# Kernel optimization log

Measured on AMD Instinct MI355X. Metric: run time of the kernel, lower is better.

Reference implementation:

```python
import jax, jax.numpy as jnp
import numpy as np
import math

B, N, M = 4, 2048, 2048
DIM_Q = DIM_K = DIM_V = 1024
H = 16

def setup_inputs() -> dict:
    key = jax.random.key(0)
    ks = jax.random.split(key, 10)
    s = 0.02
    return {
        "Q": jax.random.normal(ks[0], (B, N, DIM_Q), jnp.float32),
        "K": jax.random.normal(ks[1], (B, M, DIM_K), jnp.float32),
        "Wq": jax.random.normal(ks[2], (DIM_V, DIM_Q), jnp.float32) * s,
        "bq": jax.random.normal(ks[3], (DIM_V,), jnp.float32) * s,
        "Wk": jax.random.normal(ks[4], (DIM_V, DIM_K), jnp.float32) * s,
        "bk": jax.random.normal(ks[5], (DIM_V,), jnp.float32) * s,
        "Wv": jax.random.normal(ks[6], (DIM_V, DIM_K), jnp.float32) * s,
        "bv": jax.random.normal(ks[7], (DIM_V,), jnp.float32) * s,
        "Wo": jax.random.normal(ks[8], (DIM_V, DIM_V), jnp.float32) * s,
        "bo": jax.random.normal(ks[9], (DIM_V,), jnp.float32) * s,
    }

def reference(Q, K, Wq, bq, Wk, bk, Wv, bv, Wo, bo):
    d = DIM_V // H  # head dim
    Qp = Q @ Wq.T + bq            # [B,N,DIM_V]
    Kp = K @ Wk.T + bk            # [B,M,DIM_V]
    Vp = K @ Wv.T + bv            # [B,M,DIM_V]
    # split heads: [B,T,H,d] -> [B,H,T,d]
    Qh = Qp.reshape(B, N, H, d).transpose(0, 2, 1, 3)
    Kh = Kp.reshape(B, M, H, d).transpose(0, 2, 1, 3)
    Vh = Vp.reshape(B, M, H, d).transpose(0, 2, 1, 3)
    # NOTE: original scales by sqrt(dim_V), not sqrt(head_dim)
    scores = jnp.einsum('bhnd,bhmd->bhnm', Qh, Kh) / math.sqrt(DIM_V)
    A = jax.nn.softmax(scores, axis=-1)
    Oh = Qh + jnp.einsum('bhnm,bhmd->bhnd', A, Vh)   # residual with projected Q
    O = Oh.transpose(0, 2, 1, 3).reshape(B, N, DIM_V)
    O = O + jax.nn.relu(O @ Wo.T + bo)
    return O
```

## Files before the change

kernel.cpp:

```cpp
#include <hip/hip_runtime.h>
#include <cstddef>
#include <cstdint>


typedef unsigned short ushort_t;
typedef __attribute__((ext_vector_type(8))) short bf16x8;
typedef __attribute__((ext_vector_type(4))) float floatx4;
typedef __attribute__((ext_vector_type(8))) unsigned short us8;
typedef __attribute__((ext_vector_type(4))) unsigned short us4;

__device__ __forceinline__ ushort_t f2bf(float x) {
  union { float f; unsigned u; } v; v.f = x;
  unsigned r = v.u + 0x7FFFu + ((v.u >> 16) & 1u);
  return (ushort_t)(r >> 16);
}
__device__ __forceinline__ float bf2f(ushort_t x) {
  union { unsigned u; float f; } v; v.u = ((unsigned)x) << 16;
  return v.f;
}
__device__ __forceinline__ unsigned pk2(float a, float b) {
  union { float f; unsigned u; } x, y; x.f = a; y.f = b;
  return __builtin_amdgcn_perm(y.u + 0x8000u, x.u + 0x8000u, 0x07060302u);
}
__device__ __forceinline__ floatx4 mfma16(bf16x8 a, bf16x8 b, floatx4 c) {
  return __builtin_amdgcn_mfma_f32_16x16x32_bf16(a, b, c, 0, 0, 0);
}
__device__ __forceinline__ void gld_lds16(const void* g, void* l) {
  __builtin_amdgcn_global_load_lds(
      (const __attribute__((address_space(1))) unsigned int*)g,
      (__attribute__((address_space(3))) unsigned int*)l, 16, 0, 0);
}

__global__ void cvt4(const float* __restrict__ i0, const float* __restrict__ i1,
                     const float* __restrict__ i2, const float* __restrict__ i3,
                     ushort_t* __restrict__ o0, ushort_t* __restrict__ o1,
                     ushort_t* __restrict__ o2, ushort_t* __restrict__ o3, int n8) {
  int z = blockIdx.z;
  const float* in = z == 0 ? i0 : z == 1 ? i1 : z == 2 ? i2 : i3;
  ushort_t* out = z == 0 ? o0 : z == 1 ? o1 : z == 2 ? o2 : o3;
  int i = blockIdx.x * 256 + threadIdx.x;
  if (i < n8) {
    const float4* p = (const float4*)in + (size_t)i * 2;
    float4 a = p[0], b = p[1];
    uint4 o;
    o.x = pk2(a.x, a.y); o.y = pk2(a.z, a.w);
    o.z = pk2(b.x, b.y); o.w = pk2(b.z, b.w);
    *((uint4*)out + i) = o;
  }
}

__global__ __launch_bounds__(256, 2)
void gemm_qkv(const ushort_t* __restrict__ Qb, const ushort_t* __restrict__ Kb,
              const ushort_t* __restrict__ Wqb, const ushort_t* __restrict__ Wkb,
              const ushort_t* __restrict__ Wvb,
              const float* __restrict__ bq, const float* __restrict__ bk,
              const float* __restrict__ bv,
              ushort_t* __restrict__ Qp, ushort_t* __restrict__ Kp,
              ushort_t* __restrict__ Vt)
{
  const int Kd = 1024, Nn = 1024;
  const int z = blockIdx.z;
  const ushort_t* Ab = (z == 0) ? Qb : Kb;
  const ushort_t* Bw = (z == 0) ? Wqb : (z == 1) ? Wkb : Wvb;
  const float* bias  = (z == 0) ? bq : (z == 1) ? bk : bv;

  __shared__ __align__(16) ushort_t As[128][64];
  __shared__ __align__(16) ushort_t Bs[128][64];
  const int tid = threadIdx.x;
  const int lane = tid & 63, wave = tid >> 6;
  const int wm = (wave >> 1) * 64, wn = (wave & 1) * 64;
  const int rq = lane & 15, kg = lane >> 4;
  const int row0 = blockIdx.y * 128, col0 = blockIdx.x * 128;

  const int st_sub = lane >> 3;
  const int st_cs  = (lane & 7) ^ st_sub;

  floatx4 acc[4][4];
#pragma unroll
  for (int i = 0; i < 4; ++i)
#pragma unroll
    for (int j = 0; j < 4; ++j) acc[i][j] = (floatx4){0.f, 0.f, 0.f, 0.f};

  for (int k0 = 0; k0 < Kd; k0 += 64) {
    __syncthreads();
#pragma unroll
    for (int r = 0; r < 4; ++r) {
      int i = wave * 4 + r;
      int row = i * 8 + st_sub;
      gld_lds16(Ab + (size_t)(row0 + row) * Kd + k0 + st_cs * 8, (ushort_t*)As + i * 512);
      gld_lds16(Bw + (size_t)(col0 + row) * Kd + k0 + st_cs * 8, (ushort_t*)Bs + i * 512);
    }
    __syncthreads();
#pragma unroll
    for (int kq = 0; kq < 2; ++kq) {
      bf16x8 af[4], bfr[4];
#pragma unroll
      for (int mi = 0; mi < 4; ++mi)
        af[mi] = *(const bf16x8*)&As[wm + mi*16 + rq][((kq*4 + kg) ^ (rq & 7)) * 8];
#pragma unroll
      for (int ni = 0; ni < 4; ++ni)
        bfr[ni] = *(const bf16x8*)&Bs[wn + ni*16 + rq][((kq*4 + kg) ^ (rq & 7)) * 8];
#pragma unroll
      for (int mi = 0; mi < 4; ++mi)
#pragma unroll
        for (int ni = 0; ni < 4; ++ni)
          acc[mi][ni] = mfma16(af[mi], bfr[ni], acc[mi][ni]);
    }
  }

  float bv4[4];
#pragma unroll
  for (int ni = 0; ni < 4; ++ni) bv4[ni] = bias[col0 + wn + ni*16 + rq];

  if (z < 2) {
    ushort_t* Cb = (z == 0) ? Qp : Kp;
#pragma unroll
    for (int mi = 0; mi < 4; ++mi)
#pragma unroll
      for (int ni = 0; ni < 4; ++ni)
#pragma unroll
        for (int rr = 0; rr < 4; ++rr) {
          int row = row0 + wm + mi*16 + kg*4 + rr;
          int col = col0 + wn + ni*16 + rq;
          Cb[(size_t)row * Nn + col] = f2bf(acc[mi][ni][rr] + bv4[ni]);
        }
  } else {
#pragma unroll
    for (int mi = 0; mi < 4; ++mi)
#pragma unroll
      for (int ni = 0; ni < 4; ++ni) {
        int col = col0 + wn + ni*16 + rq;
        int base32 = row0 + wm + (mi >> 1) * 32;
        int p = kg * 8 + (mi & 1) * 4;
        us4 o = { f2bf(acc[mi][ni][0] + bv4[ni]), f2bf(acc[mi][ni][1] + bv4[ni]),
                  f2bf(acc[mi][ni][2] + bv4[ni]), f2bf(acc[mi][ni][3] + bv4[ni]) };
        *(us4*)(Vt + (size_t)col * 8192 + base32 + p) = o;
      }
  }
}

__global__ __launch_bounds__(256, 2)
void gemm_out(const ushort_t* __restrict__ Ob, const ushort_t* __restrict__ Bw,
              const float* __restrict__ bias, float* __restrict__ Out)
{
  const int Kd = 1024, Nn = 1024;
  __shared__ __align__(16) ushort_t As[128][64];
  __shared__ __align__(16) ushort_t Bs[128][64];
  const int tid = threadIdx.x;
  const int lane = tid & 63, wave = tid >> 6;
  const int wm = (wave >> 1) * 64, wn = (wave & 1) * 64;
  const int rq = lane & 15, kg = lane >> 4;
  const int row0 = blockIdx.y * 128, col0 = blockIdx.x * 128;

  const int st_sub = lane >> 3;
  const int st_cs  = (lane & 7) ^ st_sub;

  floatx4 acc[4][4];
#pragma unroll
  for (int i = 0; i < 4; ++i)
#pragma unroll
    for (int j = 0; j < 4; ++j) acc[i][j] = (floatx4){0.f, 0.f, 0.f, 0.f};

  for (int k0 = 0; k0 < Kd; k0 += 64) {
    __syncthreads();
#pragma unroll
    for (int r = 0; r < 4; ++r) {
      int i = wave * 4 + r;
      int row = i * 8 + st_sub;
      gld_lds16(Ob + (size_t)(row0 + row) * Kd + k0 + st_cs * 8, (ushort_t*)As + i * 512);
      gld_lds16(Bw + (size_t)(col0 + row) * Kd + k0 + st_cs * 8, (ushort_t*)Bs + i * 512);
    }
    __syncthreads();
#pragma unroll
    for (int kq = 0; kq < 2; ++kq) {
      bf16x8 af[4], bfr[4];
#pragma unroll
      for (int mi = 0; mi < 4; ++mi)
        af[mi] = *(const bf16x8*)&As[wm + mi*16 + rq][((kq*4 + kg) ^ (rq & 7)) * 8];
#pragma unroll
      for (int ni = 0; ni < 4; ++ni)
        bfr[ni] = *(const bf16x8*)&Bs[wn + ni*16 + rq][((kq*4 + kg) ^ (rq & 7)) * 8];
#pragma unroll
      for (int mi = 0; mi < 4; ++mi)
#pragma unroll
        for (int ni = 0; ni < 4; ++ni)
          acc[mi][ni] = mfma16(af[mi], bfr[ni], acc[mi][ni]);
    }
  }

  float bv4[4];
#pragma unroll
  for (int ni = 0; ni < 4; ++ni) bv4[ni] = bias[col0 + wn + ni*16 + rq];
#pragma unroll
  for (int mi = 0; mi < 4; ++mi)
#pragma unroll
    for (int ni = 0; ni < 4; ++ni)
#pragma unroll
      for (int rr = 0; rr < 4; ++rr) {
        int row = row0 + wm + mi*16 + kg*4 + rr;
        int col = col0 + wn + ni*16 + rq;
        size_t idx = (size_t)row * Nn + col;
        float pre = acc[mi][ni][rr] + bv4[ni];
        Out[idx] = bf2f(Ob[idx]) + (pre > 0.f ? pre : 0.f);
      }
}

__global__ __launch_bounds__(256, 2)
void attn_kernel(const ushort_t* __restrict__ Qp,
                 const ushort_t* __restrict__ Kp,
                 const ushort_t* __restrict__ Vt,
                 ushort_t* __restrict__ Ob)
{
  const float sc2 = 0.045084439f;
  const int qt = blockIdx.x;
  const int bh = blockIdx.y;
  const int b = bh >> 4, h = bh & 15;
  const int q0 = qt * 128;

  __shared__ __align__(16) ushort_t Ks[8192];
  __shared__ __align__(16) ushort_t Vs[8192];
  __shared__ float reds[128];

  const int tid = threadIdx.x, lane = tid & 63, wq = tid >> 6;
  const int rq = lane & 15, kg = lane >> 4;

  const size_t qkbase = (size_t)(b * 2048) * 1024 + h * 64;

#pragma unroll
  for (int r = 0; r < 4; ++r) {
    int i = wq * 4 + r;
    int row = i * 8 + (lane >> 3);
    int cs = (lane & 7) ^ (lane >> 3);
    gld_lds16(Qp + qkbase + (size_t)(q0 + row) * 1024 + cs * 8, Ks + i * 512);
  }
  __syncthreads();

  bf16x8 aq[2][2];
#pragma unroll
  for (int ni = 0; ni < 2; ++ni)
#pragma unroll
    for (int kq = 0; kq < 2; ++kq) {
      int row = wq * 32 + ni * 16 + rq;
      int ch = (kq * 4 + kg) ^ (rq & 7);
      bf16x8 t = *(const bf16x8*)&Ks[row * 64 + ch * 8];
#pragma unroll
      for (int e = 0; e < 8; ++e)
        t[e] = (short)f2bf(bf2f((ushort_t)t[e]) * sc2);
      aq[ni][kq] = t;
    }

  floatx4 oacc[2][4];
  float l_st[2] = {0.f, 0.f};
#pragma unroll
  for (int nb = 0; nb < 2; ++nb)
#pragma unroll
    for (int dvb = 0; dvb < 4; ++dvb) oacc[nb][dvb] = (floatx4){0.f,0.f,0.f,0.f};

  for (int kt = 0; kt < 16; ++kt) {
    const int kv0 = kt * 128;
    __syncthreads();
#pragma unroll
    for (int r = 0; r < 4; ++r) {
      int i = wq * 4 + r;
      int rowk = i * 8 + (lane >> 3);
      int csk = (lane & 7) ^ (lane >> 3);
      gld_lds16(Kp + qkbase + (size_t)(kv0 + rowk) * 1024 + csk * 8, Ks + i * 512);
      int dv = i * 4 + (lane >> 4);
      int csv = (lane & 15) ^ (dv & 7);
      gld_lds16(Vt + (size_t)(h * 64 + dv) * 8192 + b * 2048 + kv0 + csv * 8,
                Vs + i * 512);
    }
    __syncthreads();

    floatx4 s[8][2];
#pragma unroll
    for (int mi = 0; mi < 8; ++mi) {
      s[mi][0] = (floatx4){0.f,0.f,0.f,0.f};
      s[mi][1] = (floatx4){0.f,0.f,0.f,0.f};
    }
    __builtin_amdgcn_s_setprio(1);
#pragma unroll
    for (int kq = 0; kq < 2; ++kq) {
      bf16x8 ak[8];
#pragma unroll
      for (int mi = 0; mi < 8; ++mi)
        ak[mi] = *(const bf16x8*)&Ks[(mi * 16 + rq) * 64 + (((kq * 4 + kg) ^ (rq & 7)) * 8)];
#pragma unroll
      for (int mi = 0; mi < 8; ++mi)
#pragma unroll
        for (int ni = 0; ni < 2; ++ni)
          s[mi][ni] = mfma16(ak[mi], aq[ni][kq], s[mi][ni]);
    }
    __builtin_amdgcn_s_setprio(0);

#pragma unroll
    for (int mi = 0; mi < 8; ++mi)
#pragma unroll
      for (int ni = 0; ni < 2; ++ni)
#pragma unroll
        for (int rr = 0; rr < 4; ++rr)
          s[mi][ni][rr] = __builtin_amdgcn_exp2f(s[mi][ni][rr]);
#pragma unroll
    for (int ni = 0; ni < 2; ++ni) {
      float t = 0.f;
#pragma unroll
      for (int mi = 0; mi < 8; ++mi)
        t += (s[mi][ni][0] + s[mi][ni][1]) + (s[mi][ni][2] + s[mi][ni][3]);
      l_st[ni] += t;
    }

    __builtin_amdgcn_s_setprio(1);
#pragma unroll
    for (int c = 0; c < 4; ++c) {
      bf16x8 vf[4];
#pragma unroll
      for (int dvb = 0; dvb < 4; ++dvb) {
        int dv = dvb * 16 + rq;
        int ch = (c * 4 + kg) ^ (rq & 7);
        vf[dvb] = *(const bf16x8*)&Vs[dv * 128 + ch * 8];
      }
#pragma unroll
      for (int nb = 0; nb < 2; ++nb) {
        union { unsigned u[4]; bf16x8 v; } pa;
        pa.u[0] = pk2(s[2*c  ][nb][0], s[2*c  ][nb][1]);
        pa.u[1] = pk2(s[2*c  ][nb][2], s[2*c  ][nb][3]);
        pa.u[2] = pk2(s[2*c+1][nb][0], s[2*c+1][nb][1]);
        pa.u[3] = pk2(s[2*c+1][nb][2], s[2*c+1][nb][3]);
#pragma unroll
        for (int dvb = 0; dvb < 4; ++dvb)
          oacc[nb][dvb] = mfma16(pa.v, vf[dvb], oacc[nb][dvb]);
      }
    }
    __builtin_amdgcn_s_setprio(0);
  }

#pragma unroll
  for (int ni = 0; ni < 2; ++ni) {
    l_st[ni] += __shfl_xor(l_st[ni], 16, 64);
    l_st[ni] += __shfl_xor(l_st[ni], 32, 64);
  }
  if (lane < 16) {
    reds[wq * 32 + rq]      = l_st[0];
    reds[wq * 32 + 16 + rq] = l_st[1];
  }
  __syncthreads();

#pragma unroll
  for (int nb = 0; nb < 2; ++nb)
#pragma unroll
    for (int rr = 0; rr < 4; ++rr) {
      int row = wq * 32 + nb * 16 + kg * 4 + rr;
      float linv = 1.0f / reds[row];
#pragma unroll
      for (int dvb = 0; dvb < 4; ++dvb) {
        int col = dvb * 16 + rq;
        size_t idx = qkbase + (size_t)(q0 + row) * 1024 + col;
        Ob[idx] = f2bf(oacc[nb][dvb][rr] * linv + bf2f(Qp[idx]));
      }
    }
}

extern "C" void kernel_launch(void* const* d_in, const int* in_sizes, int n_in,
                              void* d_out, int out_size, void* d_ws, size_t ws_size,
                              hipStream_t stream)
{
  const float* Q  = (const float*)d_in[0];
  const float* K  = (const float*)d_in[1];
  const float* Wq = (const float*)d_in[2];
  const float* bq = (const float*)d_in[3];
  const float* Wk = (const float*)d_in[4];
  const float* bk = (const float*)d_in[5];
  const float* Wv = (const float*)d_in[6];
  const float* bv = (const float*)d_in[7];
  const float* Wo = (const float*)d_in[8];
  const float* bo = (const float*)d_in[9];
  float* Out = (float*)d_out;

  ushort_t* ws = (ushort_t*)d_ws;
  const size_t E = (size_t)8192 * 1024;
  const size_t WSZ = (size_t)1024 * 1024;
  ushort_t* Qb  = ws;
  ushort_t* Kb  = ws + E;
  ushort_t* Qp  = ws + 2*E;
  ushort_t* Kp  = ws + 3*E;
  ushort_t* Vt  = ws + 4*E;
  ushort_t* Wqb = ws + 5*E;
  ushort_t* Wkb = ws + 5*E + WSZ;
  ushort_t* Wvb = ws + 5*E + 2*WSZ;
  ushort_t* Wob = ws + 5*E + 3*WSZ;
  ushort_t* Ob  = Qb;

  cvt4<<<dim3(4096, 1, 2), 256, 0, stream>>>(Q, K, K, K, Qb, Kb, Kb, Kb, 1048576);
  cvt4<<<dim3(512, 1, 4), 256, 0, stream>>>(Wq, Wk, Wv, Wo, Wqb, Wkb, Wvb, Wob, 131072);

  dim3 blk(256);
  gemm_qkv<<<dim3(8, 64, 3), blk, 0, stream>>>(Qb, Kb, Wqb, Wkb, Wvb,
                                               bq, bk, bv, Qp, Kp, Vt);
  attn_kernel<<<dim3(16, 64), blk, 0, stream>>>(Qp, Kp, Vt, Ob);
  gemm_out<<<dim3(8, 64), blk, 0, stream>>>(Ob, Wob, bo, Out);
}
```

Baseline: 313.0 us.

## Double-buffer K/V tiles in LDS to overlap loads with attention compute

The attention kernel now keeps two LDS buffers each for K and V. It issues the global-to-LDS loads for the next KV tile before computing on the current one, so there is one barrier per iteration instead of two. The Q tile is staged through the second K buffer while the first KV tile is prefetched. The aim is to hide global memory latency behind the MFMA and exp work. The cost is doubled LDS use, which could limit occupancy alongside the two-blocks-per-CU launch bound.

```diff
diff --git a/kernel.cpp b/kernel.cpp
--- a/kernel.cpp
+++ b/kernel.cpp
@@ -217,8 +217,8 @@
   const int b = bh >> 4, h = bh & 15;
   const int q0 = qt * 128;
 
-  __shared__ __align__(16) ushort_t Ks[8192];
-  __shared__ __align__(16) ushort_t Vs[8192];
+  __shared__ __align__(16) ushort_t Ks[2][8192];
+  __shared__ __align__(16) ushort_t Vs[2][8192];
   __shared__ float reds[128];
 
   const int tid = threadIdx.x, lane = tid & 63, wq = tid >> 6;
@@ -226,14 +226,32 @@
 
   const size_t qkbase = (size_t)(b * 2048) * 1024 + h * 64;
 
+  const int sg_sub = lane >> 3;
+  const int sg_csk = (lane & 7) ^ sg_sub;
+
 #pragma unroll
   for (int r = 0; r < 4; ++r) {
     int i = wq * 4 + r;
-    int row = i * 8 + (lane >> 3);
-    int cs = (lane & 7) ^ (lane >> 3);
-    gld_lds16(Qp + qkbase + (size_t)(q0 + row) * 1024 + cs * 8, Ks + i * 512);
+    int row = i * 8 + sg_sub;
+    gld_lds16(Qp + qkbase + (size_t)(q0 + row) * 1024 + sg_csk * 8, &Ks[1][i * 512]);
   }
   __syncthreads();
+
+  auto stage = [&](int kt, int bufi) {
+    const int kv0 = kt * 128;
+#pragma unroll
+    for (int r = 0; r < 4; ++r) {
+      int i = wq * 4 + r;
+      int rowk = i * 8 + sg_sub;
+      gld_lds16(Kp + qkbase + (size_t)(kv0 + rowk) * 1024 + sg_csk * 8,
+                &Ks[bufi][i * 512]);
+      int dv = i * 4 + (lane >> 4);
+      int csv = (lane & 15) ^ (dv & 7);
+      gld_lds16(Vt + (size_t)(h * 64 + dv) * 8192 + b * 2048 + kv0 + csv * 8,
+                &Vs[bufi][i * 512]);
+    }
+  };
+  stage(0, 0);
 
   bf16x8 aq[2][2];
 #pragma unroll
@@ -242,7 +260,7 @@
     for (int kq = 0; kq < 2; ++kq) {
       int row = wq * 32 + ni * 16 + rq;
       int ch = (kq * 4 + kg) ^ (rq & 7);
-      bf16x8 t = *(const bf16x8*)&Ks[row * 64 + ch * 8];
+      bf16x8 t = *(const bf16x8*)&Ks[1][row * 64 + ch * 8];
 #pragma unroll
       for (int e = 0; e < 8; ++e)
         t[e] = (short)f2bf(bf2f((ushort_t)t[e]) * sc2);
@@ -256,21 +274,12 @@
 #pragma unroll
     for (int dvb = 0; dvb < 4; ++dvb) oacc[nb][dvb] = (floatx4){0.f,0.f,0.f,0.f};
 
+  __syncthreads();
+
+  int cur = 0;
+#pragma unroll 2
   for (int kt = 0; kt < 16; ++kt) {
-    const int kv0 = kt * 128;
-    __syncthreads();
-#pragma unroll
-    for (int r = 0; r < 4; ++r) {
-      int i = wq * 4 + r;
-      int rowk = i * 8 + (lane >> 3);
-      int csk = (lane & 7) ^ (lane >> 3);
-      gld_lds16(Kp + qkbase + (size_t)(kv0 + rowk) * 1024 + csk * 8, Ks + i * 512);
-      int dv = i * 4 + (lane >> 4);
-      int csv = (lane & 15) ^ (dv & 7);
-      gld_lds16(Vt + (size_t)(h * 64 + dv) * 8192 + b * 2048 + kv0 + csv * 8,
-                Vs + i * 512);
-    }
-    __syncthreads();
+    if (kt < 15) stage(kt + 1, cur ^ 1);
 
     floatx4 s[8][2];
 #pragma unroll
@@ -284,7 +293,7 @@
       bf16x8 ak[8];
 #pragma unroll
       for (int mi = 0; mi < 8; ++mi)
-        ak[mi] = *(const bf16x8*)&Ks[(mi * 16 + rq) * 64 + (((kq * 4 + kg) ^ (rq & 7)) * 8)];
+        ak[mi] = *(const bf16x8*)&Ks[cur][(mi * 16 + rq) * 64 + (((kq * 4 + kg) ^ (rq & 7)) * 8)];
 #pragma unroll
       for (int mi = 0; mi < 8; ++mi)
 #pragma unroll
@@ -317,7 +326,7 @@
       for (int dvb = 0; dvb < 4; ++dvb) {
         int dv = dvb * 16 + rq;
         int ch = (c * 4 + kg) ^ (rq & 7);
-        vf[dvb] = *(const bf16x8*)&Vs[dv * 128 + ch * 8];
+        vf[dvb] = *(const bf16x8*)&Vs[cur][dv * 128 + ch * 8];
       }
 #pragma unroll
       for (int nb = 0; nb < 2; ++nb) {
@@ -332,6 +341,9 @@
       }
     }
     __builtin_amdgcn_s_setprio(0);
+
+    __syncthreads();
+    cur ^= 1;
   }
 
 #pragma unroll
```

Result: no change. 308.9 us (-1.3%).
